# Kernel optimization log

Hardware: AMD Instinct MI355X
Metric: run time of the kernel (lower is better)

The kernel has to match this reference:

```python
import jax, jax.numpy as jnp
import numpy as np

D = 8
W = 256
NUM_FREQS = 10
NUM_FREQS_VIEWS = 4
SKIPS = (4,)
PE_DIM = 3 + 2 * 3 * NUM_FREQS        # 63
VE_DIM = 3 + 2 * 3 * NUM_FREQS_VIEWS  # 27
N_RAYS, N_SAMPLES = 4096, 64


def embed(x, num_freqs):
    # torch order: [x, sin(x*f0), cos(x*f0), sin(x*f1), cos(x*f1), ...]
    freqs = (2.0 ** jnp.arange(num_freqs)).astype(x.dtype)
    xf = x[..., None, :] * freqs[:, None]              # [..., F, 3]
    sc = jnp.stack([jnp.sin(xf), jnp.cos(xf)], axis=-2)  # [..., F, 2, 3]
    return jnp.concatenate([x, sc.reshape(*x.shape[:-1], num_freqs * 6)], -1)


def setup_inputs() -> dict:
    key = jax.random.key(0)
    ks = iter(jax.random.split(key, 32))
    inp = {}
    inp["input_pts"] = jax.random.normal(next(ks), (N_RAYS, N_SAMPLES, 3), jnp.float32)
    inp["input_views"] = jax.random.normal(next(ks), (N_RAYS, 3), jnp.float32)
    # pts MLP: layer 5 (index 5) takes W + PE_DIM due to skip after layer 4
    in_dims = [PE_DIM] + [(W + PE_DIM) if i in SKIPS else W for i in range(D - 1)]
    for i, d in enumerate(in_dims):
        inp[f"pts_w{i}"] = jax.random.normal(next(ks), (d, W), jnp.float32) / np.sqrt(d).astype(np.float32)
        inp[f"pts_b{i}"] = jnp.zeros((W,), jnp.float32)
    inp["views_w"] = jax.random.normal(next(ks), (VE_DIM + W, W // 2), jnp.float32) / np.sqrt(VE_DIM + W).astype(np.float32)
    inp["views_b"] = jnp.zeros((W // 2,), jnp.float32)
    inp["feat_w"] = jax.random.normal(next(ks), (W, W), jnp.float32) / np.sqrt(W).astype(np.float32)
    inp["feat_b"] = jnp.zeros((W,), jnp.float32)
    inp["alpha_w"] = jax.random.normal(next(ks), (W, 1), jnp.float32) / np.sqrt(W).astype(np.float32)
    inp["alpha_b"] = jnp.zeros((1,), jnp.float32)
    inp["rgb_w"] = jax.random.normal(next(ks), (W // 2, 3), jnp.float32) / np.sqrt(W // 2).astype(np.float32)
    inp["rgb_b"] = jnp.zeros((3,), jnp.float32)
    return inp


def reference(input_pts, input_views,
              pts_w0, pts_b0, pts_w1, pts_b1, pts_w2, pts_b2, pts_w3, pts_b3,
              pts_w4, pts_b4, pts_w5, pts_b5, pts_w6, pts_b6, pts_w7, pts_b7,
              views_w, views_b, feat_w, feat_b, alpha_w, alpha_b, rgb_w, rgb_b):
    pts_ws = [pts_w0, pts_w1, pts_w2, pts_w3, pts_w4, pts_w5, pts_w6, pts_w7]
    pts_bs = [pts_b0, pts_b1, pts_b2, pts_b3, pts_b4, pts_b5, pts_b6, pts_b7]
    R, S = input_pts.shape[0], input_pts.shape[1]
    ep = embed(input_pts, NUM_FREQS).reshape(-1, PE_DIM)            # [R*S, 63]
    ev = embed(input_views, NUM_FREQS_VIEWS)                        # [R, 27]
    ev = jnp.broadcast_to(ev[:, None, :], (R, S, VE_DIM)).reshape(-1, VE_DIM)
    h = ep
    for i in range(D):
        h = jax.nn.relu(h @ pts_ws[i] + pts_bs[i])
        if i in SKIPS:
            h = jnp.concatenate([ep, h], -1)
    alpha = h @ alpha_w + alpha_b                                    # [R*S, 1]
    feature = h @ feat_w + feat_b                                    # [R*S, W]
    h2 = jax.nn.relu(jnp.concatenate([feature, ev], -1) @ views_w + views_b)
    rgb = h2 @ rgb_w + rgb_b                                         # [R*S, 3]
    return jnp.concatenate([rgb, alpha], -1).reshape(R, S, 4)
```

## Files before the change

### kernel.cpp

```cpp
#include <hip/hip_runtime.h>

typedef _Float16 h16;
typedef __attribute__((ext_vector_type(8))) _Float16 half8;
typedef __attribute__((ext_vector_type(4))) float f32x4;

#define LDH 264
#define LDE 72

constexpr size_t OFF_P0 = 0;
constexpr size_t OFF_P1 = 16384;
constexpr size_t OFF_P2 = 81920;
constexpr size_t OFF_P3 = 147456;
constexpr size_t OFF_P4 = 212992;
constexpr size_t OFF_P5 = 278528;
constexpr size_t OFF_P6 = 360448;
constexpr size_t OFF_P7 = 425984;
constexpr size_t OFF_FEAT = 491520;
constexpr size_t OFF_VIEWS = 557056;

__device__ __forceinline__ f32x4 mfma16(half8 a, half8 b, f32x4 c) {
  return __builtin_amdgcn_mfma_f32_16x16x32_f16(a, b, c, 0, 0, 0);
}

__global__ void convw_kernel(const float* __restrict__ src, h16* __restrict__ dst,
                             int Ksrc, int N, int Kp, int p, int npad) {
  int t = blockIdx.x * 256 + threadIdx.x;
  int nfrags = (Kp >> 5) * (N >> 4);
  int frag = t >> 6;
  if (frag >= nfrags) return;
  int l = t & 63;
  int ntiles = N >> 4;
  int kt = frag / ntiles;
  int nt = frag - kt * ntiles;
  int col = nt * 16 + (l & 15);
  int kbase = kt * 32 + (l >> 4) * 8;
  half8 v;
#pragma unroll
  for (int j = 0; j < 8; ++j) {
    int k = kbase + j;
    float x = 0.f;
    if (k < p) {
      x = src[(size_t)k * N + col];
    } else if (k >= p + npad) {
      int r = k - npad;
      if (r < Ksrc) x = src[(size_t)r * N + col];
    }
    v[j] = (h16)x;
  }
  *(half8*)(dst + (size_t)frag * 512 + (size_t)l * 8) = v;
}

struct Params {
  const float* pts;
  const float* views;
  const h16* wf;
  const float* pb[8];
  const float* views_b;
  const float* feat_b;
  const float* alpha_w;
  const float* alpha_b;
  const float* rgb_w;
  const float* rgb_b;
  float* out;
};

template <int KT, int KT0, bool RELU>
__device__ __forceinline__ void gemm256(const h16* __restrict__ src0, int ld0,
                                        const h16* __restrict__ src1, int ld1,
                                        const h16* __restrict__ wf,
                                        const float* __restrict__ bias,
                                        h16* __restrict__ dst,
                                        int w, int lrow, int lgrp, int l) {
  f32x4 acc[4][4];
  const f32x4 z = {0.f, 0.f, 0.f, 0.f};
#pragma unroll
  for (int mt = 0; mt < 4; ++mt)
#pragma unroll
    for (int nt = 0; nt < 4; ++nt) acc[mt][nt] = z;

#pragma unroll
  for (int kt = 0; kt < KT; ++kt) {
    half8 a[4];
#pragma unroll
    for (int mt = 0; mt < 4; ++mt) {
      const h16* ap;
      if (kt < KT0) ap = src0 + (size_t)(mt * 16 + lrow) * ld0 + kt * 32 + lgrp * 8;
      else          ap = src1 + (size_t)(mt * 16 + lrow) * ld1 + (kt - KT0) * 32 + lgrp * 8;
      a[mt] = *(const half8*)ap;
    }
    half8 b[4];
#pragma unroll
    for (int nt = 0; nt < 4; ++nt)
      b[nt] = *(const half8*)(wf + ((size_t)(kt * 16 + w * 4 + nt) * 64 + l) * 8);
#pragma unroll
    for (int mt = 0; mt < 4; ++mt)
#pragma unroll
      for (int nt = 0; nt < 4; ++nt)
        acc[mt][nt] = mfma16(a[mt], b[nt], acc[mt][nt]);
  }
#pragma unroll
  for (int nt = 0; nt < 4; ++nt) {
    int col = w * 64 + nt * 16 + lrow;
    float bv = bias[col];
#pragma unroll
    for (int mt = 0; mt < 4; ++mt) {
#pragma unroll
      for (int i = 0; i < 4; ++i) {
        float v = acc[mt][nt][i] + bv;
        if (RELU) v = fmaxf(v, 0.f);
        dst[(size_t)(mt * 16 + lgrp * 4 + i) * LDH + col] = (h16)v;
      }
    }
  }
}

__device__ __forceinline__ void gemm128(const h16* __restrict__ feat,
                                        const h16* __restrict__ evp,
                                        const h16* __restrict__ wf,
                                        const float* __restrict__ bias,
                                        h16* __restrict__ dst,
                                        int w, int lrow, int lgrp, int l) {
  f32x4 acc[4][2];
  const f32x4 z = {0.f, 0.f, 0.f, 0.f};
#pragma unroll
  for (int mt = 0; mt < 4; ++mt) { acc[mt][0] = z; acc[mt][1] = z; }

#pragma unroll
  for (int kt = 0; kt < 9; ++kt) {
    half8 a[4];
    if (kt < 8) {
#pragma unroll
      for (int mt = 0; mt < 4; ++mt)
        a[mt] = *(const half8*)(feat + (size_t)(mt * 16 + lrow) * LDH + kt * 32 + lgrp * 8);
    } else {
      half8 av = *(const half8*)(evp + lgrp * 8);
#pragma unroll
      for (int mt = 0; mt < 4; ++mt) a[mt] = av;
    }
    half8 b[2];
#pragma unroll
    for (int nt = 0; nt < 2; ++nt)
      b[nt] = *(const half8*)(wf + ((size_t)(kt * 8 + w * 2 + nt) * 64 + l) * 8);
#pragma unroll
    for (int mt = 0; mt < 4; ++mt)
#pragma unroll
      for (int nt = 0; nt < 2; ++nt)
        acc[mt][nt] = mfma16(a[mt], b[nt], acc[mt][nt]);
  }
#pragma unroll
  for (int nt = 0; nt < 2; ++nt) {
    int col = w * 32 + nt * 16 + lrow;
    float bv = bias[col];
#pragma unroll
    for (int mt = 0; mt < 4; ++mt) {
#pragma unroll
      for (int i = 0; i < 4; ++i) {
        float v = fmaxf(acc[mt][nt][i] + bv, 0.f);
        dst[(size_t)(mt * 16 + lgrp * 4 + i) * LDH + col] = (h16)v;
      }
    }
  }
}

__global__ __launch_bounds__(256, 2) void nerf_kernel(Params P) {
  __shared__ __align__(16) h16 ep[64 * LDE];
  __shared__ __align__(16) h16 hA[64 * LDH];
  __shared__ __align__(16) h16 hB[64 * LDH];
  __shared__ __align__(16) h16 evp[32];
  __shared__ float alpha_s[64];

  const int tid = threadIdx.x;
  const int w = tid >> 6, l = tid & 63;
  const int lrow = l & 15, lgrp = l >> 4;
  const int ray = blockIdx.x;

  if (tid < 64) {
    const int s = tid;
    const float x0 = P.pts[((size_t)ray * 64 + s) * 3 + 0];
    const float x1 = P.pts[((size_t)ray * 64 + s) * 3 + 1];
    const float x2 = P.pts[((size_t)ray * 64 + s) * 3 + 2];
    h16* e = ep + (size_t)s * LDE;
    e[0] = (h16)x0; e[1] = (h16)x1; e[2] = (h16)x2;
#pragma unroll
    for (int f = 0; f < 10; ++f) {
      const float sc = (float)(1 << f);
      e[3 + 6 * f + 0] = (h16)sinf(x0 * sc);
      e[3 + 6 * f + 1] = (h16)sinf(x1 * sc);
      e[3 + 6 * f + 2] = (h16)sinf(x2 * sc);
      e[3 + 6 * f + 3] = (h16)cosf(x0 * sc);
      e[3 + 6 * f + 4] = (h16)cosf(x1 * sc);
      e[3 + 6 * f + 5] = (h16)cosf(x2 * sc);
    }
    e[63] = (h16)0.f;
  } else if (tid < 96) {
    const int idx = tid - 64;
    float v = 0.f;
    if (idx < 27) {
      if (idx < 3) {
        v = P.views[(size_t)ray * 3 + idx];
      } else {
        const int f = (idx - 3) / 6, rem = (idx - 3) % 6, d = rem % 3;
        const float x = P.views[(size_t)ray * 3 + d] * (float)(1 << f);
        v = (rem < 3) ? sinf(x) : cosf(x);
      }
    }
    evp[idx] = (h16)v;
  }
  __syncthreads();

  gemm256<2, 2, true>(ep, LDE, ep, LDE, P.wf + OFF_P0, P.pb[0], hA, w, lrow, lgrp, l);
  __syncthreads();
  gemm256<8, 0, true>(ep, LDE, hA, LDH, P.wf + OFF_P1, P.pb[1], hB, w, lrow, lgrp, l);
  __syncthreads();
  gemm256<8, 0, true>(ep, LDE, hB, LDH, P.wf + OFF_P2, P.pb[2], hA, w, lrow, lgrp, l);
  __syncthreads();
  gemm256<8, 0, true>(ep, LDE, hA, LDH, P.wf + OFF_P3, P.pb[3], hB, w, lrow, lgrp, l);
  __syncthreads();
  gemm256<8, 0, true>(ep, LDE, hB, LDH, P.wf + OFF_P4, P.pb[4], hA, w, lrow, lgrp, l);
  __syncthreads();
  gemm256<10, 2, true>(ep, LDE, hA, LDH, P.wf + OFF_P5, P.pb[5], hB, w, lrow, lgrp, l);
  __syncthreads();
  gemm256<8, 0, true>(ep, LDE, hB, LDH, P.wf + OFF_P6, P.pb[6], hA, w, lrow, lgrp, l);
  __syncthreads();
  gemm256<8, 0, true>(ep, LDE, hA, LDH, P.wf + OFF_P7, P.pb[7], hB, w, lrow, lgrp, l);
  __syncthreads();

  {
    const int s = tid >> 2, q = tid & 3;
    float sum = 0.f;
#pragma unroll 8
    for (int k = 0; k < 64; ++k)
      sum += (float)hB[(size_t)s * LDH + q * 64 + k] * P.alpha_w[q * 64 + k];
    sum += __shfl_xor(sum, 1);
    sum += __shfl_xor(sum, 2);
    if (q == 0) alpha_s[s] = sum + P.alpha_b[0];
  }

  gemm256<8, 0, false>(ep, LDE, hB, LDH, P.wf + OFF_FEAT, P.feat_b, hA, w, lrow, lgrp, l);
  __syncthreads();

  gemm128(hA, evp, P.wf + OFF_VIEWS, P.views_b, hB, w, lrow, lgrp, l);
  __syncthreads();

  {
    const int s = tid >> 2, q = tid & 3;
    float r0 = 0.f, r1 = 0.f, r2 = 0.f;
#pragma unroll 8
    for (int k = 0; k < 32; ++k) {
      const int kk = q * 32 + k;
      const float h = (float)hB[(size_t)s * LDH + kk];
      r0 += h * P.rgb_w[kk * 3 + 0];
      r1 += h * P.rgb_w[kk * 3 + 1];
      r2 += h * P.rgb_w[kk * 3 + 2];
    }
    r0 += __shfl_xor(r0, 1); r0 += __shfl_xor(r0, 2);
    r1 += __shfl_xor(r1, 1); r1 += __shfl_xor(r1, 2);
    r2 += __shfl_xor(r2, 1); r2 += __shfl_xor(r2, 2);
    if (q == 0) {
      float4 o;
      o.x = r0 + P.rgb_b[0];
      o.y = r1 + P.rgb_b[1];
      o.z = r2 + P.rgb_b[2];
      o.w = alpha_s[s];
      *(float4*)(P.out + ((size_t)ray * 64 + s) * 4) = o;
    }
  }
}

extern "C" void kernel_launch(void* const* d_in, const int* in_sizes, int n_in,
                              void* d_out, int out_size, void* d_ws, size_t ws_size,
                              hipStream_t stream) {
  h16* wsw = (h16*)d_ws;
  auto conv = [&](int idx, int Ksrc, int N, int Kp, int p, int npad, size_t off) {
    int nfrags = (Kp / 32) * (N / 16);
    int total = nfrags * 64;
    convw_kernel<<<(total + 255) / 256, 256, 0, stream>>>(
        (const float*)d_in[idx], wsw + off, Ksrc, N, Kp, p, npad);
  };
  conv(2, 63, 256, 64, 63, 1, OFF_P0);
  conv(4, 256, 256, 256, 256, 0, OFF_P1);
  conv(6, 256, 256, 256, 256, 0, OFF_P2);
  conv(8, 256, 256, 256, 256, 0, OFF_P3);
  conv(10, 256, 256, 256, 256, 0, OFF_P4);
  conv(12, 319, 256, 320, 63, 1, OFF_P5);
  conv(14, 256, 256, 256, 256, 0, OFF_P6);
  conv(16, 256, 256, 256, 256, 0, OFF_P7);
  conv(20, 256, 256, 256, 256, 0, OFF_FEAT);
  conv(18, 283, 128, 288, 283, 5, OFF_VIEWS);

  Params P;
  P.pts = (const float*)d_in[0];
  P.views = (const float*)d_in[1];
  P.wf = wsw;
  for (int i = 0; i < 8; ++i) P.pb[i] = (const float*)d_in[3 + 2 * i];
  P.views_b = (const float*)d_in[19];
  P.feat_b = (const float*)d_in[21];
  P.alpha_w = (const float*)d_in[22];
  P.alpha_b = (const float*)d_in[23];
  P.rgb_w = (const float*)d_in[24];
  P.rgb_b = (const float*)d_in[25];
  P.out = (float*)d_out;

  nerf_kernel<<<4096, 256, 0, stream>>>(P);
}
```

Before: 393.2 us.

## Use single in-place LDS activation buffer and vectorized transposed epilogue stores

The two ping-pong LDS activation buffers are merged into one buffer updated in place. A barrier between the MFMA loop and the epilogue keeps the in-place writes safe, and launch bounds rise to 3 blocks per SIMD group to use the freed LDS. MFMA operands are swapped so each lane holds 4 consecutive output columns, which allows packed half4 stores and a vector bias load instead of scalar strided writes. In exchange, every layer pays an extra block barrier, and the tighter launch bound may constrain registers for the 64-float accumulator tile.

```diff
diff --git a/kernel.cpp b/kernel.cpp
--- a/kernel.cpp
+++ b/kernel.cpp
@@ -2,6 +2,7 @@
 
 typedef _Float16 h16;
 typedef __attribute__((ext_vector_type(8))) _Float16 half8;
+typedef __attribute__((ext_vector_type(4))) _Float16 half4;
 typedef __attribute__((ext_vector_type(4))) float f32x4;
 
 #define LDH 264
@@ -64,7 +65,7 @@
   float* out;
 };
 
-template <int KT, int KT0, bool RELU>
+template <int KT, int KT0, bool RELU, bool PRE_BAR>
 __device__ __forceinline__ void gemm256(const h16* __restrict__ src0, int ld0,
                                         const h16* __restrict__ src1, int ld1,
                                         const h16* __restrict__ wf,
@@ -96,22 +97,27 @@
     for (int mt = 0; mt < 4; ++mt)
 #pragma unroll
       for (int nt = 0; nt < 4; ++nt)
-        acc[mt][nt] = mfma16(a[mt], b[nt], acc[mt][nt]);
-  }
-#pragma unroll
-  for (int nt = 0; nt < 4; ++nt) {
-    int col = w * 64 + nt * 16 + lrow;
-    float bv = bias[col];
-#pragma unroll
-    for (int mt = 0; mt < 4; ++mt) {
+        acc[mt][nt] = mfma16(b[nt], a[mt], acc[mt][nt]);
+  }
+  if (PRE_BAR) __syncthreads();
+#pragma unroll
+  for (int mt = 0; mt < 4; ++mt) {
+    int row = mt * 16 + lrow;
+#pragma unroll
+    for (int nt = 0; nt < 4; ++nt) {
+      int col0 = w * 64 + nt * 16 + lgrp * 4;
+      f32x4 bv = *(const f32x4*)(bias + col0);
+      half4 pk;
 #pragma unroll
       for (int i = 0; i < 4; ++i) {
-        float v = acc[mt][nt][i] + bv;
+        float v = acc[mt][nt][i] + bv[i];
         if (RELU) v = fmaxf(v, 0.f);
-        dst[(size_t)(mt * 16 + lgrp * 4 + i) * LDH + col] = (h16)v;
+        pk[i] = (h16)v;
       }
-    }
-  }
+      *(half4*)(dst + (size_t)row * LDH + col0) = pk;
+    }
+  }
+  __syncthreads();
 }
 
 __device__ __forceinline__ void gemm128(const h16* __restrict__ feat,
@@ -145,27 +151,29 @@
     for (int mt = 0; mt < 4; ++mt)
 #pragma unroll
       for (int nt = 0; nt < 2; ++nt)
-        acc[mt][nt] = mfma16(a[mt], b[nt], acc[mt][nt]);
-  }
-#pragma unroll
-  for (int nt = 0; nt < 2; ++nt) {
-    int col = w * 32 + nt * 16 + lrow;
-    float bv = bias[col];
-#pragma unroll
-    for (int mt = 0; mt < 4; ++mt) {
-#pragma unroll
-      for (int i = 0; i < 4; ++i) {
-        float v = fmaxf(acc[mt][nt][i] + bv, 0.f);
-        dst[(size_t)(mt * 16 + lgrp * 4 + i) * LDH + col] = (h16)v;
-      }
-    }
-  }
-}
-
-__global__ __launch_bounds__(256, 2) void nerf_kernel(Params P) {
+        acc[mt][nt] = mfma16(b[nt], a[mt], acc[mt][nt]);
+  }
+  __syncthreads();
+#pragma unroll
+  for (int mt = 0; mt < 4; ++mt) {
+    int row = mt * 16 + lrow;
+#pragma unroll
+    for (int nt = 0; nt < 2; ++nt) {
+      int col0 = w * 32 + nt * 16 + lgrp * 4;
+      f32x4 bv = *(const f32x4*)(bias + col0);
+      half4 pk;
+#pragma unroll
+      for (int i = 0; i < 4; ++i)
+        pk[i] = (h16)fmaxf(acc[mt][nt][i] + bv[i], 0.f);
+      *(half4*)(dst + (size_t)row * LDH + col0) = pk;
+    }
+  }
+  __syncthreads();
+}
+
+__global__ __launch_bounds__(256, 3) void nerf_kernel(Params P) {
   __shared__ __align__(16) h16 ep[64 * LDE];
-  __shared__ __align__(16) h16 hA[64 * LDH];
-  __shared__ __align__(16) h16 hB[64 * LDH];
+  __shared__ __align__(16) h16 h[64 * LDH];
   __shared__ __align__(16) h16 evp[32];
   __shared__ float alpha_s[64];
 
@@ -208,39 +216,29 @@
   }
   __syncthreads();
 
-  gemm256<2, 2, true>(ep, LDE, ep, LDE, P.wf + OFF_P0, P.pb[0], hA, w, lrow, lgrp, l);
-  __syncthreads();
-  gemm256<8, 0, true>(ep, LDE, hA, LDH, P.wf + OFF_P1, P.pb[1], hB, w, lrow, lgrp, l);
-  __syncthreads();
-  gemm256<8, 0, true>(ep, LDE, hB, LDH, P.wf + OFF_P2, P.pb[2], hA, w, lrow, lgrp, l);
-  __syncthreads();
-  gemm256<8, 0, true>(ep, LDE, hA, LDH, P.wf + OFF_P3, P.pb[3], hB, w, lrow, lgrp, l);
-  __syncthreads();
-  gemm256<8, 0, true>(ep, LDE, hB, LDH, P.wf + OFF_P4, P.pb[4], hA, w, lrow, lgrp, l);
-  __syncthreads();
-  gemm256<10, 2, true>(ep, LDE, hA, LDH, P.wf + OFF_P5, P.pb[5], hB, w, lrow, lgrp, l);
-  __syncthreads();
-  gemm256<8, 0, true>(ep, LDE, hB, LDH, P.wf + OFF_P6, P.pb[6], hA, w, lrow, lgrp, l);
-  __syncthreads();
-  gemm256<8, 0, true>(ep, LDE, hA, LDH, P.wf + OFF_P7, P.pb[7], hB, w, lrow, lgrp, l);
-  __syncthreads();
+  gemm256<2, 2, true, false>(ep, LDE, ep, LDE, P.wf + OFF_P0, P.pb[0], h, w, lrow, lgrp, l);
+  gemm256<8, 0, true, true>(ep, LDE, h, LDH, P.wf + OFF_P1, P.pb[1], h, w, lrow, lgrp, l);
+  gemm256<8, 0, true, true>(ep, LDE, h, LDH, P.wf + OFF_P2, P.pb[2], h, w, lrow, lgrp, l);
+  gemm256<8, 0, true, true>(ep, LDE, h, LDH, P.wf + OFF_P3, P.pb[3], h, w, lrow, lgrp, l);
+  gemm256<8, 0, true, true>(ep, LDE, h, LDH, P.wf + OFF_P4, P.pb[4], h, w, lrow, lgrp, l);
+  gemm256<10, 2, true, true>(ep, LDE, h, LDH, P.wf + OFF_P5, P.pb[5], h, w, lrow, lgrp, l);
+  gemm256<8, 0, true, true>(ep, LDE, h, LDH, P.wf + OFF_P6, P.pb[6], h, w, lrow, lgrp, l);
+  gemm256<8, 0, true, true>(ep, LDE, h, LDH, P.wf + OFF_P7, P.pb[7], h, w, lrow, lgrp, l);
 
   {
     const int s = tid >> 2, q = tid & 3;
     float sum = 0.f;
 #pragma unroll 8
     for (int k = 0; k < 64; ++k)
-      sum += (float)hB[(size_t)s * LDH + q * 64 + k] * P.alpha_w[q * 64 + k];
+      sum += (float)h[(size_t)s * LDH + q * 64 + k] * P.alpha_w[q * 64 + k];
     sum += __shfl_xor(sum, 1);
     sum += __shfl_xor(sum, 2);
     if (q == 0) alpha_s[s] = sum + P.alpha_b[0];
   }
 
-  gemm256<8, 0, false>(ep, LDE, hB, LDH, P.wf + OFF_FEAT, P.feat_b, hA, w, lrow, lgrp, l);
-  __syncthreads();
-
-  gemm128(hA, evp, P.wf + OFF_VIEWS, P.views_b, hB, w, lrow, lgrp, l);
-  __syncthreads();
+  gemm256<8, 0, false, true>(ep, LDE, h, LDH, P.wf + OFF_FEAT, P.feat_b, h, w, lrow, lgrp, l);
+
+  gemm128(h, evp, P.wf + OFF_VIEWS, P.views_b, h, w, lrow, lgrp, l);
 
   {
     const int s = tid >> 2, q = tid & 3;
@@ -248,10 +246,10 @@
 #pragma unroll 8
     for (int k = 0; k < 32; ++k) {
       const int kk = q * 32 + k;
-      const float h = (float)hB[(size_t)s * LDH + kk];
-      r0 += h * P.rgb_w[kk * 3 + 0];
-      r1 += h * P.rgb_w[kk * 3 + 1];
-      r2 += h * P.rgb_w[kk * 3 + 2];
+      const float hv = (float)h[(size_t)s * LDH + kk];
+      r0 += hv * P.rgb_w[kk * 3 + 0];
+      r1 += hv * P.rgb_w[kk * 3 + 1];
+      r2 += hv * P.rgb_w[kk * 3 + 2];
     }
     r0 += __shfl_xor(r0, 1); r0 += __shfl_xor(r0, 2);
     r1 += __shfl_xor(r1, 1); r1 += __shfl_xor(r1, 2);
```

Result: slower. 458.2 us (+16.5%).
